# Kernel optimization log

Measured on AMD Instinct MI355X. Metric: run time of the kernel, lower is better.

Reference implementation:

```python
import jax, jax.numpy as jnp
import numpy as np
from jax import lax

B, S, T = 128, 1000, 256
V, E, KV, H = 30, 256, 256, 512


def setup_inputs() -> dict:
    ks = jax.random.split(jax.random.key(0), 20)
    sc = 0.1
    emb = jax.random.normal(ks[0], (V, E), jnp.float32) * sc
    emb = emb.at[29].set(0.0)  # padding_idx=29
    return {
        "enc_key": jax.random.normal(ks[1], (B, S, KV), jnp.float32),
        "value": jax.random.normal(ks[2], (B, S, KV), jnp.float32),
        "y": jax.random.randint(ks[3], (T, B), 0, V),
        "encoder_len": jax.random.randint(ks[4], (B,), 1, S + 1),
        "embedding": emb,
        "W_ih1": jax.random.normal(ks[5], (4 * H, E + KV), jnp.float32) * sc,
        "b_ih1": jax.random.normal(ks[6], (4 * H,), jnp.float32) * sc,
        "W_hh1": jax.random.normal(ks[7], (4 * H, H), jnp.float32) * sc,
        "b_hh1": jax.random.normal(ks[8], (4 * H,), jnp.float32) * sc,
        "W_ih2": jax.random.normal(ks[9], (4 * H, H), jnp.float32) * sc,
        "b_ih2": jax.random.normal(ks[10], (4 * H,), jnp.float32) * sc,
        "W_hh2": jax.random.normal(ks[11], (4 * H, H), jnp.float32) * sc,
        "b_hh2": jax.random.normal(ks[12], (4 * H,), jnp.float32) * sc,
        "Wq": jax.random.normal(ks[13], (KV, H), jnp.float32) * sc,
        "bq": jax.random.normal(ks[14], (KV,), jnp.float32) * sc,
        "Wc": jax.random.normal(ks[15], (V, 2 * KV), jnp.float32) * sc,
        "bc": jax.random.normal(ks[16], (V,), jnp.float32) * sc,
    }


def _lstm_cell(x, h, c, W_ih, b_ih, W_hh, b_hh):
    gates = x @ W_ih.T + b_ih + h @ W_hh.T + b_hh
    i, f, g, o = jnp.split(gates, 4, axis=1)
    c_new = jax.nn.sigmoid(f) * c + jax.nn.sigmoid(i) * jnp.tanh(g)
    h_new = jax.nn.sigmoid(o) * jnp.tanh(c_new)
    return h_new, c_new


def reference(enc_key, value, y, encoder_len, embedding,
              W_ih1, b_ih1, W_hh1, b_hh1,
              W_ih2, b_ih2, W_hh2, b_hh2,
              Wq, bq, Wc, bc):
    # y: [T, B] -> [B, T]; note: original computes mask from encoder_len but the
    # non-in-place masked_fill discards it, so masking has NO effect (reproduced).
    del encoder_len
    yT = y.T  # [B, T]
    b, s, kv = enc_key.shape
    scale = jnp.sqrt(jnp.asarray(s, jnp.float32))
    char_embeds = embedding[yT]          # [B, T, E]
    ctx0 = value.mean(axis=1)            # [B, KV]  (value.permute(0,2,1).mean(-1))
    h = W_hh1.shape[1]
    z = jnp.zeros((b, h), enc_key.dtype)

    def step(carry, e_t):
        h1, c1, h2, c2, ctx = carry
        x = jnp.concatenate([e_t, ctx], axis=1)                 # [B, E+KV]
        h1n, c1n = _lstm_cell(x, h1, c1, W_ih1, b_ih1, W_hh1, b_hh1)
        # original feeds lstm1's CELL state into lstm2 (hidden_states[0][1])
        h2n, c2n = _lstm_cell(c1n, h2, c2, W_ih2, b_ih2, W_hh2, b_hh2)
        # query from lstm2's CELL state (hidden_states[1][1])
        q = c2n @ Wq.T + bq                                     # [B, KV]
        energy = (jnp.einsum('bsk,bk->bs', enc_key, q) + 1e-9) / scale
        attn = jax.nn.softmax(energy, axis=1)                   # [B, S]
        ctxn = jnp.einsum('bsk,bs->bk', value, attn)            # [B, KV]
        pred = jnp.concatenate([ctxn, q], axis=1) @ Wc.T + bc   # [B, V]
        return (h1n, c1n, h2n, c2n, ctxn), (pred, attn[0])

    _, (preds, attn0) = lax.scan(step, (z, z, z, z, ctx0),
                                 jnp.swapaxes(char_embeds, 0, 1))
    predictions = jnp.transpose(preds, (1, 0, 2)).reshape(b, -1)  # [B, T*V] (cat dim=1)
    attentions = attn0[..., None]                                 # [T, S, 1]
    return predictions, attentions
```

## Files before the change

### kernel.cpp

```cpp
#include <hip/hip_runtime.h>
#include <hip/hip_bf16.h>

#define NB 128
#define NS 1000
#define NT 256
#define NV 30
#define NE 256
#define NKV 256
#define NH 512
#define NG 2048
#define NK 1024

typedef __hip_bfloat16 bf;
typedef unsigned short ushortT;

__device__ __forceinline__ float sigm(float x){ return 1.f/(1.f+__expf(-x)); }
__device__ __forceinline__ float tanh_fast(float x){ float e=__expf(2.f*x); return 1.f - 2.f/(e+1.f); }
__device__ __forceinline__ float bf2f(ushortT u){ return __uint_as_float(((unsigned)u)<<16); }
__device__ __forceinline__ void bf8_to_f(const ushortT* p, float* o){
  uint4 u = *reinterpret_cast<const uint4*>(p);
  o[0]=__uint_as_float(u.x<<16); o[1]=__uint_as_float(u.x&0xffff0000u);
  o[2]=__uint_as_float(u.y<<16); o[3]=__uint_as_float(u.y&0xffff0000u);
  o[4]=__uint_as_float(u.z<<16); o[5]=__uint_as_float(u.z&0xffff0000u);
  o[6]=__uint_as_float(u.w<<16); o[7]=__uint_as_float(u.w&0xffff0000u);
}
__device__ __forceinline__ float ldDual(const void* p, size_t i, bool bfm){
  return bfm ? bf2f(((const ushortT*)p)[i]) : ((const float*)p)[i];
}

__global__ void k_probe(const unsigned* __restrict__ x, unsigned* __restrict__ flag){
  __shared__ int cnt;
  if (threadIdx.x==0) cnt = 0;
  __syncthreads();
  int c = 0;
  #pragma unroll
  for (int i=0;i<4;++i){
    unsigned d = x[(size_t)threadIdx.x*4 + i];
    unsigned e = (d >> 7) & 0xffu;
    c += (e >= 119 && e <= 135) ? 1 : 0;
  }
  atomicAdd(&cnt, c);
  __syncthreads();
  if (threadIdx.x==0) *flag = (cnt >= 512) ? 1u : 0u;
}

__global__ void k_wtp(const void* __restrict__ A, const void* __restrict__ Bm,
                      float* __restrict__ Wtp, const unsigned* __restrict__ flag){
  const bool bfm = (*flag != 0);
  int idx = blockIdx.x*256 + threadIdx.x;
  int k = idx >> 11, pc = idx & (NG-1);
  int j = pc >> 2, g = pc & 3;
  int col = g*NH + j;
  const void* p = (k < NH) ? A : Bm;
  Wtp[idx] = ldDual(p, (size_t)col*NH + (k & (NH-1)), bfm);
}

__global__ void k_biasp(const void* bi1, const void* bh1, const void* bi2, const void* bh2,
                        float* __restrict__ bsum1, float* __restrict__ bsum2,
                        const unsigned* __restrict__ flag){
  const bool bfm = (*flag != 0);
  int idx = blockIdx.x*256 + threadIdx.x;
  int which = idx >= NG; int pc = idx & (NG-1);
  int j = pc >> 2, g = pc & 3;
  int col = g*NH + j;
  const void* a = which ? bi2 : bi1;
  const void* c = which ? bh2 : bh1;
  float v = ldDual(a, col, bfm) + ldDual(c, col, bfm);
  (which ? bsum2 : bsum1)[pc] = v;
}

__global__ void k_init(const void* __restrict__ value, const int* __restrict__ y,
                       const void* __restrict__ emb,
                       float* __restrict__ X1a, float* __restrict__ X2a,
                       float* __restrict__ c1, float* __restrict__ c2,
                       const unsigned* __restrict__ flag){
  const bool bfm = (*flag != 0);
  int b = blockIdx.x, tid = threadIdx.x;
  float acc = 0.f;
  if (bfm){
    const ushortT* vcol = (const ushortT*)value + (size_t)b*NS*NKV + tid;
    for (int s=0;s<NS;++s) acc += bf2f(vcol[(size_t)s*NKV]);
  } else {
    const float* vcol = (const float*)value + (size_t)b*NS*NKV + tid;
    for (int s=0;s<NS;++s) acc += vcol[(size_t)s*NKV];
  }
  X1a[(size_t)b*NK + NE + tid] = acc * (1.f/NS);
  int yv = y[b];
  X1a[(size_t)b*NK + tid] = ldDual(emb, (size_t)yv*NE + tid, bfm);
  X1a[(size_t)b*NK + 512 + tid] = 0.f; X1a[(size_t)b*NK + 768 + tid] = 0.f;
  X2a[(size_t)b*NK + 512 + tid] = 0.f; X2a[(size_t)b*NK + 768 + tid] = 0.f;
  c1[(size_t)b*NH + tid] = 0.f; c1[(size_t)b*NH + 256 + tid] = 0.f;
  c2[(size_t)b*NH + tid] = 0.f; c2[(size_t)b*NH + 256 + tid] = 0.f;
}

__global__ __launch_bounds__(512) void k_lstm(
    const float* __restrict__ X, const float* __restrict__ Wtp,
    const float* __restrict__ bsump,
    float* __restrict__ cstate,
    float* __restrict__ outC, int outCstride, int hasC,
    float* __restrict__ outH)
{
  const int i = blockIdx.x;
  const int cb = ((i & 7) << 3) | ((i >> 3) & 7);
  const int rb = i >> 6;
  const int r0 = rb * 32;
  const int pc0 = cb * 32;
  const int tid = threadIdx.x;
  const int khalf = tid >> 8;
  const int t8 = tid & 255;
  const int rp = t8 >> 4;
  const int cp = t8 & 15;
  __shared__ float Xs[2][64][33];
  __shared__ float redbuf[256][4];
  __shared__ float gbuf[32][33];

  float a00=0.f, a01=0.f, a10=0.f, a11=0.f;
  const int kbase = khalf * 512;
  const int sr  = t8 >> 4;
  const int sk4 = (t8 & 15) * 4;

  for (int cch = 0; cch < 8; ++cch){
    __syncthreads();
    {
      const float4 v0 = *reinterpret_cast<const float4*>(
          X + (size_t)(r0+sr)*NK + kbase + cch*64 + sk4);
      const float4 v1 = *reinterpret_cast<const float4*>(
          X + (size_t)(r0+sr+16)*NK + kbase + cch*64 + sk4);
      Xs[khalf][sk4+0][sr]    = v0.x; Xs[khalf][sk4+1][sr]    = v0.y;
      Xs[khalf][sk4+2][sr]    = v0.z; Xs[khalf][sk4+3][sr]    = v0.w;
      Xs[khalf][sk4+0][sr+16] = v1.x; Xs[khalf][sk4+1][sr+16] = v1.y;
      Xs[khalf][sk4+2][sr+16] = v1.z; Xs[khalf][sk4+3][sr+16] = v1.w;
    }
    __syncthreads();
    const float* wp = Wtp + (size_t)(kbase + cch*64)*NG + pc0 + cp*2;
    #pragma unroll 8
    for (int kk=0; kk<64; ++kk){
      const float2 w = *reinterpret_cast<const float2*>(wp + (size_t)kk*NG);
      const float2 x = *reinterpret_cast<const float2*>(&Xs[khalf][kk][rp*2]);
      a00 = fmaf(x.x, w.x, a00); a01 = fmaf(x.x, w.y, a01);
      a10 = fmaf(x.y, w.x, a10); a11 = fmaf(x.y, w.y, a11);
    }
  }
  if (khalf == 1){
    redbuf[t8][0]=a00; redbuf[t8][1]=a01; redbuf[t8][2]=a10; redbuf[t8][3]=a11;
  }
  __syncthreads();
  if (khalf == 0){
    a00 += redbuf[t8][0]; a01 += redbuf[t8][1];
    a10 += redbuf[t8][2]; a11 += redbuf[t8][3];
    gbuf[rp*2+0][cp*2+0]=a00; gbuf[rp*2+0][cp*2+1]=a01;
    gbuf[rp*2+1][cp*2+0]=a10; gbuf[rp*2+1][cp*2+1]=a11;
  }
  __syncthreads();
  if (tid < 256){
    const int er = tid >> 3;
    const int jj = tid & 7;
    const int r = r0 + er;
    const int jg = cb*8 + jj;
    const int pb = pc0 + jj*4;
    float iv = gbuf[er][jj*4+0] + bsump[pb+0];
    float fv = gbuf[er][jj*4+1] + bsump[pb+1];
    float gv = gbuf[er][jj*4+2] + bsump[pb+2];
    float ov = gbuf[er][jj*4+3] + bsump[pb+3];
    float cold = cstate[(size_t)r*NH + jg];
    float cn = sigm(fv)*cold + sigm(iv)*tanh_fast(gv);
    float hn = sigm(ov)*tanh_fast(cn);
    cstate[(size_t)r*NH + jg] = cn;
    if (hasC) outC[(size_t)r*outCstride + jg] = cn;
    outH[(size_t)r*NK + jg] = hn;
  }
}

__global__ __launch_bounds__(512) void k_attn(
    const float* __restrict__ c2, const void* __restrict__ Wq, const void* __restrict__ bq,
    const void* __restrict__ key, const void* __restrict__ val,
    const void* __restrict__ Wc, const void* __restrict__ bc,
    const int* __restrict__ y, const void* __restrict__ emb,
    float* __restrict__ X1next, void* __restrict__ outp,
    const unsigned* __restrict__ flag, int t)
{
  const bool bfm = (*flag != 0);
  const int b = blockIdx.x, tid = threadIdx.x, lane = tid & 63, wave = tid >> 6;
  __shared__ float c2s[NH];
  __shared__ float qs[NKV];
  __shared__ float ps[NS];
  __shared__ float ctxs[NKV];
  __shared__ float red[16];
  __shared__ float psum[NV][17];
  __shared__ float ctxpart[8][NKV];

  c2s[tid] = c2[(size_t)b*NH + tid];
  __syncthreads();

  if (tid < NKV){
    float qacc = ldDual(bq, tid, bfm);
    if (bfm){
      const ushortT* wrow = (const ushortT*)Wq + (size_t)tid*NH;
      #pragma unroll 4
      for (int j=0;j<NH;j+=8){
        float wv[8]; bf8_to_f(wrow + j, wv);
        #pragma unroll
        for (int u=0;u<8;++u) qacc = fmaf(wv[u], c2s[j+u], qacc);
      }
    } else {
      const float4* wrow = reinterpret_cast<const float4*>((const float*)Wq + (size_t)tid*NH);
      #pragma unroll 4
      for (int j4=0; j4<NH/4; ++j4){
        float4 w = wrow[j4]; int j = j4*4;
        qacc = fmaf(w.x, c2s[j+0], qacc); qacc = fmaf(w.y, c2s[j+1], qacc);
        qacc = fmaf(w.z, c2s[j+2], qacc); qacc = fmaf(w.w, c2s[j+3], qacc);
      }
    }
    qs[tid] = qacc;
  }
  __syncthreads();

  const int k0 = (lane & 15)*16;
  float qreg[16];
  #pragma unroll
  for (int u=0;u<16;++u) qreg[u] = qs[k0+u];
  const float rscale = 0.031622776601683794f;
  for (int s0 = wave*8; s0 < NS; s0 += 64){
    int sA = s0 + (lane >> 4);
    int sB = sA + 4;
    float aA = 0.f, aB = 0.f;
    if (bfm){
      if (sA < NS){
        const ushortT* kp = (const ushortT*)key + ((size_t)b*NS + sA)*NKV + k0;
        float xv[8];
        bf8_to_f(kp, xv);
        #pragma unroll
        for (int u=0;u<8;++u) aA = fmaf(xv[u], qreg[u], aA);
        bf8_to_f(kp + 8, xv);
        #pragma unroll
        for (int u=0;u<8;++u) aA = fmaf(xv[u], qreg[8+u], aA);
      }
      if (sB < NS){
        const ushortT* kp = (const ushortT*)key + ((size_t)b*NS + sB)*NKV + k0;
        float xv[8];
        bf8_to_f(kp, xv);
        #pragma unroll
        for (int u=0;u<8;++u) aB = fmaf(xv[u], qreg[u], aB);
        bf8_to_f(kp + 8, xv);
        #pragma unroll
        for (int u=0;u<8;++u) aB = fmaf(xv[u], qreg[8+u], aB);
      }
    } else {
      const float* kA = (const float*)key + ((size_t)b*NS + sA)*NKV + k0;
      const float* kB = (const float*)key + ((size_t)b*NS + sB)*NKV + k0;
      float4 a0,a1,a2,a3, b0,b1,b2,b3;
      bool gA = (sA < NS), gB = (sB < NS);
      if (gA){
        a0 = *reinterpret_cast<const float4*>(kA);
        a1 = *reinterpret_cast<const float4*>(kA+4);
        a2 = *reinterpret_cast<const float4*>(kA+8);
        a3 = *reinterpret_cast<const float4*>(kA+12);
      }
      if (gB){
        b0 = *reinterpret_cast<const float4*>(kB);
        b1 = *reinterpret_cast<const float4*>(kB+4);
        b2 = *reinterpret_cast<const float4*>(kB+8);
        b3 = *reinterpret_cast<const float4*>(kB+12);
      }
      if (gA){
        aA = fmaf(a0.x,qreg[0],aA); aA = fmaf(a0.y,qreg[1],aA);
        aA = fmaf(a0.z,qreg[2],aA); aA = fmaf(a0.w,qreg[3],aA);
        aA = fmaf(a1.x,qreg[4],aA); aA = fmaf(a1.y,qreg[5],aA);
        aA = fmaf(a1.z,qreg[6],aA); aA = fmaf(a1.w,qreg[7],aA);
        aA = fmaf(a2.x,qreg[8],aA); aA = fmaf(a2.y,qreg[9],aA);
        aA = fmaf(a2.z,qreg[10],aA); aA = fmaf(a2.w,qreg[11],aA);
        aA = fmaf(a3.x,qreg[12],aA); aA = fmaf(a3.y,qreg[13],aA);
        aA = fmaf(a3.z,qreg[14],aA); aA = fmaf(a3.w,qreg[15],aA);
      }
      if (gB){
        aB = fmaf(b0.x,qreg[0],aB); aB = fmaf(b0.y,qreg[1],aB);
        aB = fmaf(b0.z,qreg[2],aB); aB = fmaf(b0.w,qreg[3],aB);
        aB = fmaf(b1.x,qreg[4],aB); aB = fmaf(b1.y,qreg[5],aB);
        aB = fmaf(b1.z,qreg[6],aB); aB = fmaf(b1.w,qreg[7],aB);
        aB = fmaf(b2.x,qreg[8],aB); aB = fmaf(b2.y,qreg[9],aB);
        aB = fmaf(b2.z,qreg[10],aB); aB = fmaf(b2.w,qreg[11],aB);
        aB = fmaf(b3.x,qreg[12],aB); aB = fmaf(b3.y,qreg[13],aB);
        aB = fmaf(b3.z,qreg[14],aB); aB = fmaf(b3.w,qreg[15],aB);
      }
    }
    aA += __shfl_xor(aA,1); aA += __shfl_xor(aA,2);
    aA += __shfl_xor(aA,4); aA += __shfl_xor(aA,8);
    aB += __shfl_xor(aB,1); aB += __shfl_xor(aB,2);
    aB += __shfl_xor(aB,4); aB += __shfl_xor(aB,8);
    if ((lane & 15) == 0){
      if (sA < NS) ps[sA] = (aA + 1e-9f)*rscale;
      if (sB < NS) ps[sB] = (aB + 1e-9f)*rscale;
    }
  }
  __syncthreads();

  float m = -1e30f;
  for (int s=tid; s<NS; s+=512) m = fmaxf(m, ps[s]);
  #pragma unroll
  for (int d=1; d<64; d<<=1) m = fmaxf(m, __shfl_xor(m, d));
  if (lane == 0) red[wave] = m;
  __syncthreads();
  m = red[0];
  #pragma unroll
  for (int w=1; w<8; ++w) m = fmaxf(m, red[w]);
  float sum = 0.f;
  for (int s=tid; s<NS; s+=512){ float p = __expf(ps[s]-m); ps[s] = p; sum += p; }
  #pragma unroll
  for (int d=1; d<64; d<<=1) sum += __shfl_xor(sum, d);
  if (lane == 0) red[8+wave] = sum;
  __syncthreads();
  sum = red[8];
  #pragma unroll
  for (int w=1; w<8; ++w) sum += red[8+w];
  const float invS = 1.f/sum;

  const size_t ATTN_OFF = (size_t)NB*NT*NV;
  if (b == 0){
    for (int s=tid; s<NS; s+=512){
      float v = ps[s]*invS;
      if (bfm) ((bf*)outp)[ATTN_OFF + (size_t)t*NS + s] = __float2bfloat16(v);
      else     ((float*)outp)[ATTN_OFF + (size_t)t*NS + s] = v;
    }
  }

  {
    float ca[8] = {0.f,0.f,0.f,0.f,0.f,0.f,0.f,0.f};
    float cb2[8] = {0.f,0.f,0.f,0.f,0.f,0.f,0.f,0.f};
    const int sset = lane >> 5;
    const int kc = (lane & 31) * 8;
    const int sst = wave*2 + sset;
    int s = sst;
    if (bfm){
      const ushortT* vbase = (const ushortT*)val + (size_t)b*NS*NKV + kc;
      for (; s + 16 < NS; s += 32){
        float p0 = ps[s], p1 = ps[s+16];
        float xv[8];
        bf8_to_f(vbase + (size_t)s*NKV, xv);
        #pragma unroll
        for (int u=0;u<8;++u) ca[u] = fmaf(xv[u], p0, ca[u]);
        bf8_to_f(vbase + (size_t)(s+16)*NKV, xv);
        #pragma unroll
        for (int u=0;u<8;++u) cb2[u] = fmaf(xv[u], p1, cb2[u]);
      }
      if (s < NS){
        float p0 = ps[s];
        float xv[8]; bf8_to_f(vbase + (size_t)s*NKV, xv);
        #pragma unroll
        for (int u=0;u<8;++u) ca[u] = fmaf(xv[u], p0, ca[u]);
      }
    } else {
      const float* vbase = (const float*)val + (size_t)b*NS*NKV + kc;
      for (; s + 16 < NS; s += 32){
        float p0 = ps[s], p1 = ps[s+16];
        const float4 v0 = *reinterpret_cast<const float4*>(vbase + (size_t)s*NKV);
        const float4 v1 = *reinterpret_cast<const float4*>(vbase + (size_t)s*NKV + 4);
        const float4 w0 = *reinterpret_cast<const float4*>(vbase + (size_t)(s+16)*NKV);
        const float4 w1 = *reinterpret_cast<const float4*>(vbase + (size_t)(s+16)*NKV + 4);
        ca[0]=fmaf(v0.x,p0,ca[0]); ca[1]=fmaf(v0.y,p0,ca[1]);
        ca[2]=fmaf(v0.z,p0,ca[2]); ca[3]=fmaf(v0.w,p0,ca[3]);
        ca[4]=fmaf(v1.x,p0,ca[4]); ca[5]=fmaf(v1.y,p0,ca[5]);
        ca[6]=fmaf(v1.z,p0,ca[6]); ca[7]=fmaf(v1.w,p0,ca[7]);
        cb2[0]=fmaf(w0.x,p1,cb2[0]); cb2[1]=fmaf(w0.y,p1,cb2[1]);
        cb2[2]=fmaf(w0.z,p1,cb2[2]); cb2[3]=fmaf(w0.w,p1,cb2[3]);
        cb2[4]=fmaf(w1.x,p1,cb2[4]); cb2[5]=fmaf(w1.y,p1,cb2[5]);
        cb2[6]=fmaf(w1.z,p1,cb2[6]); cb2[7]=fmaf(w1.w,p1,cb2[7]);
      }
      if (s < NS){
        float p0 = ps[s];
        const float4 v0 = *reinterpret_cast<const float4*>(vbase + (size_t)s*NKV);
        const float4 v1 = *reinterpret_cast<const float4*>(vbase + (size_t)s*NKV + 4);
        ca[0]=fmaf(v0.x,p0,ca[0]); ca[1]=fmaf(v0.y,p0,ca[1]);
        ca[2]=fmaf(v0.z,p0,ca[2]); ca[3]=fmaf(v0.w,p0,ca[3]);
        ca[4]=fmaf(v1.x,p0,ca[4]); ca[5]=fmaf(v1.y,p0,ca[5]);
        ca[6]=fmaf(v1.z,p0,ca[6]); ca[7]=fmaf(v1.w,p0,ca[7]);
      }
    }
    #pragma unroll
    for (int u=0;u<8;++u){
      float v = ca[u] + cb2[u];
      v += __shfl_xor(v, 32);
      if (lane < 32) ctxpart[wave][kc+u] = v;
    }
  }
  __syncthreads();
  if (tid < NKV){
    float ctxv = 0.f;
    #pragma unroll
    for (int w=0; w<8; ++w) ctxv += ctxpart[w][tid];
    ctxv *= invS;
    ctxs[tid] = ctxv;
    X1next[(size_t)b*NK + NE + tid] = ctxv;
  }
  __syncthreads();

  {
    int vIdx = tid >> 4, part = tid & 15;
    if (vIdx < NV){
      float a = 0.f;
      int kb0 = part*32;
      for (int k=kb0; k<kb0+32; ++k){
        float xv = (k < NKV) ? ctxs[k] : qs[k-NKV];
        a = fmaf(xv, ldDual(Wc, (size_t)vIdx*(2*NKV) + k, bfm), a);
      }
      psum[vIdx][part] = a;
    }
  }
  __syncthreads();
  if (tid < NV){
    float a = ldDual(bc, tid, bfm);
    #pragma unroll
    for (int p=0;p<16;++p) a += psum[tid][p];
    size_t oi = (size_t)b*(NT*NV) + (size_t)t*NV + tid;
    if (bfm) ((bf*)outp)[oi] = __float2bfloat16(a);
    else     ((float*)outp)[oi] = a;
  }

  if (t + 1 < NT && tid < NE){
    int yv = y[(size_t)(t+1)*NB + b];
    X1next[(size_t)b*NK + tid] = ldDual(emb, (size_t)yv*NE + tid, bfm);
  }
}

extern "C" void kernel_launch(void* const* d_in, const int* in_sizes, int n_in,
                              void* d_out, int out_size, void* d_ws, size_t ws_size,
                              hipStream_t stream)
{
  const void* enc_key = d_in[0];
  const void* value   = d_in[1];
  const int*  y       = (const int*)d_in[2];
  const void* emb     = d_in[4];
  const void* W_ih1   = d_in[5];
  const void* b_ih1   = d_in[6];
  const void* W_hh1   = d_in[7];
  const void* b_hh1   = d_in[8];
  const void* W_ih2   = d_in[9];
  const void* b_ih2   = d_in[10];
  const void* W_hh2   = d_in[11];
  const void* b_hh2   = d_in[12];
  const void* Wq      = d_in[13];
  const void* bq      = d_in[14];
  const void* Wc      = d_in[15];
  const void* bc      = d_in[16];

  char* base = (char*)d_ws; size_t off = 0;
  auto alloc = [&](size_t bytes)->char*{
    char* p = base + off; off += (bytes + 255) & ~(size_t)255; return p;
  };
  float* Wtp1 = (float*)alloc((size_t)NK*NG*4);
  float* Wtp2 = (float*)alloc((size_t)NK*NG*4);
  float* bsum1 = (float*)alloc((size_t)NG*4);
  float* bsum2 = (float*)alloc((size_t)NG*4);
  float* X1[2] = {(float*)alloc((size_t)NB*NK*4), (float*)alloc((size_t)NB*NK*4)};
  float* X2[2] = {(float*)alloc((size_t)NB*NK*4), (float*)alloc((size_t)NB*NK*4)};
  float* c1 = (float*)alloc((size_t)NB*NH*4);
  float* c2 = (float*)alloc((size_t)NB*NH*4);
  unsigned* flag = (unsigned*)alloc(256);
  (void)ws_size;

  k_probe<<<1, 256, 0, stream>>>((const unsigned*)enc_key, flag);
  k_wtp<<<(NK*NG)/256, 256, 0, stream>>>(W_ih1, W_hh1, Wtp1, flag);
  k_wtp<<<(NK*NG)/256, 256, 0, stream>>>(W_ih2, W_hh2, Wtp2, flag);
  k_biasp<<<(2*NG)/256, 256, 0, stream>>>(b_ih1, b_hh1, b_ih2, b_hh2, bsum1, bsum2, flag);
  k_init<<<NB, 256, 0, stream>>>(value, y, emb, X1[0], X2[0], c1, c2, flag);

  for (int t=0; t<NT; ++t){
    int cur = t & 1, nxt = cur ^ 1;
    k_lstm<<<256, 512, 0, stream>>>(X1[cur], Wtp1, bsum1, c1,
                                    X2[cur], NK, 1, X1[nxt] + NH);
    k_lstm<<<256, 512, 0, stream>>>(X2[cur], Wtp2, bsum2, c2,
                                    nullptr, 0, 0, X2[nxt] + NH);
    k_attn<<<NB, 512, 0, stream>>>(c2, Wq, bq, enc_key, value, Wc, bc,
                                   y, emb, X1[nxt], d_out, flag, t);
  }
}
```

Before: 40.94 ms.

## Split attention over two sequence halves with flash-style softmax combine kernel

The attention step is split across two blocks per batch row, each handling half of the encoder sequence and producing a partial max, sum and unnormalised context. A new combine kernel merges the halves with log-sum-exp rescaling, then computes the output projection, the attention row and the next embedding. This doubles the blocks working on the memory-bound key/value streaming, from 128 to 256 on a GPU with many CUs. In exchange it adds one kernel launch per timestep, duplicates the query projection in both halves, and passes partial results through global memory.

```diff
diff --git a/kernel.cpp b/kernel.cpp
--- a/kernel.cpp
+++ b/kernel.cpp
@@ -3,6 +3,7 @@
 
 #define NB 128
 #define NS 1000
+#define NSH 500
 #define NT 256
 #define NV 30
 #define NE 256
@@ -171,22 +172,21 @@
   }
 }
 
-__global__ __launch_bounds__(512) void k_attn(
+__global__ __launch_bounds__(512) void k_attn_part(
     const float* __restrict__ c2, const void* __restrict__ Wq, const void* __restrict__ bq,
     const void* __restrict__ key, const void* __restrict__ val,
-    const void* __restrict__ Wc, const void* __restrict__ bc,
-    const int* __restrict__ y, const void* __restrict__ emb,
-    float* __restrict__ X1next, void* __restrict__ outp,
-    const unsigned* __restrict__ flag, int t)
+    float* __restrict__ qbuf, float* __restrict__ pctx, float* __restrict__ pstat,
+    float* __restrict__ psbuf,
+    const unsigned* __restrict__ flag)
 {
   const bool bfm = (*flag != 0);
-  const int b = blockIdx.x, tid = threadIdx.x, lane = tid & 63, wave = tid >> 6;
+  const int b = blockIdx.x >> 1, half = blockIdx.x & 1;
+  const int sbase = half * NSH;
+  const int tid = threadIdx.x, lane = tid & 63, wave = tid >> 6;
   __shared__ float c2s[NH];
   __shared__ float qs[NKV];
-  __shared__ float ps[NS];
-  __shared__ float ctxs[NKV];
+  __shared__ float ps[512];
   __shared__ float red[16];
-  __shared__ float psum[NV][17];
   __shared__ float ctxpart[8][NKV];
 
   c2s[tid] = c2[(size_t)b*NH + tid];
@@ -212,6 +212,7 @@
       }
     }
     qs[tid] = qacc;
+    if (half == 0) qbuf[(size_t)b*NKV + tid] = qacc;
   }
   __syncthreads();
 
@@ -220,13 +221,13 @@
   #pragma unroll
   for (int u=0;u<16;++u) qreg[u] = qs[k0+u];
   const float rscale = 0.031622776601683794f;
-  for (int s0 = wave*8; s0 < NS; s0 += 64){
-    int sA = s0 + (lane >> 4);
+  for (int i0 = wave*8; i0 < NSH; i0 += 64){
+    int sA = i0 + (lane >> 4);
     int sB = sA + 4;
     float aA = 0.f, aB = 0.f;
     if (bfm){
-      if (sA < NS){
-        const ushortT* kp = (const ushortT*)key + ((size_t)b*NS + sA)*NKV + k0;
+      if (sA < NSH){
+        const ushortT* kp = (const ushortT*)key + ((size_t)b*NS + sbase + sA)*NKV + k0;
         float xv[8];
         bf8_to_f(kp, xv);
         #pragma unroll
@@ -235,8 +236,8 @@
         #pragma unroll
         for (int u=0;u<8;++u) aA = fmaf(xv[u], qreg[8+u], aA);
       }
-      if (sB < NS){
-        const ushortT* kp = (const ushortT*)key + ((size_t)b*NS + sB)*NKV + k0;
+      if (sB < NSH){
+        const ushortT* kp = (const ushortT*)key + ((size_t)b*NS + sbase + sB)*NKV + k0;
         float xv[8];
         bf8_to_f(kp, xv);
         #pragma unroll
@@ -246,10 +247,10 @@
         for (int u=0;u<8;++u) aB = fmaf(xv[u], qreg[8+u], aB);
       }
     } else {
-      const float* kA = (const float*)key + ((size_t)b*NS + sA)*NKV + k0;
-      const float* kB = (const float*)key + ((size_t)b*NS + sB)*NKV + k0;
+      const float* kA = (const float*)key + ((size_t)b*NS + sbase + sA)*NKV + k0;
+      const float* kB = (const float*)key + ((size_t)b*NS + sbase + sB)*NKV + k0;
       float4 a0,a1,a2,a3, b0,b1,b2,b3;
-      bool gA = (sA < NS), gB = (sB < NS);
+      bool gA = (sA < NSH), gB = (sB < NSH);
       if (gA){
         a0 = *reinterpret_cast<const float4*>(kA);
         a1 = *reinterpret_cast<const float4*>(kA+4);
@@ -288,14 +289,14 @@
     aB += __shfl_xor(aB,1); aB += __shfl_xor(aB,2);
     aB += __shfl_xor(aB,4); aB += __shfl_xor(aB,8);
     if ((lane & 15) == 0){
-      if (sA < NS) ps[sA] = (aA + 1e-9f)*rscale;
-      if (sB < NS) ps[sB] = (aB + 1e-9f)*rscale;
+      if (sA < NSH) ps[sA] = (aA + 1e-9f)*rscale;
+      if (sB < NSH) ps[sB] = (aB + 1e-9f)*rscale;
     }
   }
   __syncthreads();
 
   float m = -1e30f;
-  for (int s=tid; s<NS; s+=512) m = fmaxf(m, ps[s]);
+  if (tid < NSH) m = ps[tid];
   #pragma unroll
   for (int d=1; d<64; d<<=1) m = fmaxf(m, __shfl_xor(m, d));
   if (lane == 0) red[wave] = m;
@@ -304,7 +305,7 @@
   #pragma unroll
   for (int w=1; w<8; ++w) m = fmaxf(m, red[w]);
   float sum = 0.f;
-  for (int s=tid; s<NS; s+=512){ float p = __expf(ps[s]-m); ps[s] = p; sum += p; }
+  if (tid < NSH){ float p = __expf(ps[tid]-m); ps[tid] = p; sum = p; }
   #pragma unroll
   for (int d=1; d<64; d<<=1) sum += __shfl_xor(sum, d);
   if (lane == 0) red[8+wave] = sum;
@@ -312,16 +313,11 @@
   sum = red[8];
   #pragma unroll
   for (int w=1; w<8; ++w) sum += red[8+w];
-  const float invS = 1.f/sum;
-
-  const size_t ATTN_OFF = (size_t)NB*NT*NV;
-  if (b == 0){
-    for (int s=tid; s<NS; s+=512){
-      float v = ps[s]*invS;
-      if (bfm) ((bf*)outp)[ATTN_OFF + (size_t)t*NS + s] = __float2bfloat16(v);
-      else     ((float*)outp)[ATTN_OFF + (size_t)t*NS + s] = v;
-    }
-  }
+  if (tid == 0){
+    pstat[((size_t)b*2 + half)*2 + 0] = m;
+    pstat[((size_t)b*2 + half)*2 + 1] = sum;
+  }
+  if (b == 0 && tid < NSH) psbuf[sbase + tid] = ps[tid];
 
   {
     float ca[8] = {0.f,0.f,0.f,0.f,0.f,0.f,0.f,0.f};
@@ -331,8 +327,8 @@
     const int sst = wave*2 + sset;
     int s = sst;
     if (bfm){
-      const ushortT* vbase = (const ushortT*)val + (size_t)b*NS*NKV + kc;
-      for (; s + 16 < NS; s += 32){
+      const ushortT* vbase = (const ushortT*)val + ((size_t)b*NS + sbase)*NKV + kc;
+      for (; s + 16 < NSH; s += 32){
         float p0 = ps[s], p1 = ps[s+16];
         float xv[8];
         bf8_to_f(vbase + (size_t)s*NKV, xv);
@@ -342,15 +338,15 @@
         #pragma unroll
         for (int u=0;u<8;++u) cb2[u] = fmaf(xv[u], p1, cb2[u]);
       }
-      if (s < NS){
+      if (s < NSH){
         float p0 = ps[s];
         float xv[8]; bf8_to_f(vbase + (size_t)s*NKV, xv);
         #pragma unroll
         for (int u=0;u<8;++u) ca[u] = fmaf(xv[u], p0, ca[u]);
       }
     } else {
-      const float* vbase = (const float*)val + (size_t)b*NS*NKV + kc;
-      for (; s + 16 < NS; s += 32){
+      const float* vbase = (const float*)val + ((size_t)b*NS + sbase)*NKV + kc;
+      for (; s + 16 < NSH; s += 32){
         float p0 = ps[s], p1 = ps[s+16];
         const float4 v0 = *reinterpret_cast<const float4*>(vbase + (size_t)s*NKV);
         const float4 v1 = *reinterpret_cast<const float4*>(vbase + (size_t)s*NKV + 4);
@@ -365,7 +361,7 @@
         cb2[4]=fmaf(w1.x,p1,cb2[4]); cb2[5]=fmaf(w1.y,p1,cb2[5]);
         cb2[6]=fmaf(w1.z,p1,cb2[6]); cb2[7]=fmaf(w1.w,p1,cb2[7]);
       }
-      if (s < NS){
+      if (s < NSH){
         float p0 = ps[s];
         const float4 v0 = *reinterpret_cast<const float4*>(vbase + (size_t)s*NKV);
         const float4 v1 = *reinterpret_cast<const float4*>(vbase + (size_t)s*NKV + 4);
@@ -387,18 +383,52 @@
     float ctxv = 0.f;
     #pragma unroll
     for (int w=0; w<8; ++w) ctxv += ctxpart[w][tid];
-    ctxv *= invS;
-    ctxs[tid] = ctxv;
-    X1next[(size_t)b*NK + NE + tid] = ctxv;
+    pctx[((size_t)b*2 + half)*NKV + tid] = ctxv;
+  }
+}
+
+__global__ __launch_bounds__(256) void k_attn_comb(
+    const float* __restrict__ qbuf, const float* __restrict__ pctx,
+    const float* __restrict__ pstat, const float* __restrict__ psbuf,
+    const void* __restrict__ Wc, const void* __restrict__ bc,
+    const int* __restrict__ y, const void* __restrict__ emb,
+    float* __restrict__ X1next, void* __restrict__ outp,
+    const unsigned* __restrict__ flag, int t)
+{
+  const bool bfm = (*flag != 0);
+  const int b = blockIdx.x, tid = threadIdx.x;
+  __shared__ float qs[NKV];
+  __shared__ float ctxs[NKV];
+  __shared__ float psum[NV][9];
+
+  const float mA = pstat[((size_t)b*2+0)*2+0], sA = pstat[((size_t)b*2+0)*2+1];
+  const float mB = pstat[((size_t)b*2+1)*2+0], sB = pstat[((size_t)b*2+1)*2+1];
+  const float m = fmaxf(mA, mB);
+  const float wA = __expf(mA - m), wB = __expf(mB - m);
+  const float invS = 1.f / (sA*wA + sB*wB);
+
+  qs[tid] = qbuf[(size_t)b*NKV + tid];
+  float ctxv = (pctx[((size_t)b*2+0)*NKV + tid]*wA +
+                pctx[((size_t)b*2+1)*NKV + tid]*wB) * invS;
+  ctxs[tid] = ctxv;
+  X1next[(size_t)b*NK + NE + tid] = ctxv;
+
+  const size_t ATTN_OFF = (size_t)NB*NT*NV;
+  if (b == 0){
+    for (int s=tid; s<NS; s+=256){
+      float v = psbuf[s] * ((s < NSH) ? wA : wB) * invS;
+      if (bfm) ((bf*)outp)[ATTN_OFF + (size_t)t*NS + s] = __float2bfloat16(v);
+      else     ((float*)outp)[ATTN_OFF + (size_t)t*NS + s] = v;
+    }
   }
   __syncthreads();
 
   {
-    int vIdx = tid >> 4, part = tid & 15;
+    int vIdx = tid >> 3, part = tid & 7;
     if (vIdx < NV){
       float a = 0.f;
-      int kb0 = part*32;
-      for (int k=kb0; k<kb0+32; ++k){
+      int kb0 = part*64;
+      for (int k=kb0; k<kb0+64; ++k){
         float xv = (k < NKV) ? ctxs[k] : qs[k-NKV];
         a = fmaf(xv, ldDual(Wc, (size_t)vIdx*(2*NKV) + k, bfm), a);
       }
@@ -409,13 +439,13 @@
   if (tid < NV){
     float a = ldDual(bc, tid, bfm);
     #pragma unroll
-    for (int p=0;p<16;++p) a += psum[tid][p];
+    for (int p=0;p<8;++p) a += psum[tid][p];
     size_t oi = (size_t)b*(NT*NV) + (size_t)t*NV + tid;
     if (bfm) ((bf*)outp)[oi] = __float2bfloat16(a);
     else     ((float*)outp)[oi] = a;
   }
 
-  if (t + 1 < NT && tid < NE){
+  if (t + 1 < NT){
     int yv = y[(size_t)(t+1)*NB + b];
     X1next[(size_t)b*NK + tid] = ldDual(emb, (size_t)yv*NE + tid, bfm);
   }
@@ -454,6 +484,10 @@
   float* X2[2] = {(float*)alloc((size_t)NB*NK*4), (float*)alloc((size_t)NB*NK*4)};
   float* c1 = (float*)alloc((size_t)NB*NH*4);
   float* c2 = (float*)alloc((size_t)NB*NH*4);
+  float* qbuf  = (float*)alloc((size_t)NB*NKV*4);
+  float* pctx  = (float*)alloc((size_t)NB*2*NKV*4);
+  float* pstat = (float*)alloc((size_t)NB*2*2*4);
+  float* psbuf = (float*)alloc((size_t)NS*4);
   unsigned* flag = (unsigned*)alloc(256);
   (void)ws_size;
 
@@ -469,7 +503,9 @@
                                     X2[cur], NK, 1, X1[nxt] + NH);
     k_lstm<<<256, 512, 0, stream>>>(X2[cur], Wtp2, bsum2, c2,
                                     nullptr, 0, 0, X2[nxt] + NH);
-    k_attn<<<NB, 512, 0, stream>>>(c2, Wq, bq, enc_key, value, Wc, bc,
-                                   y, emb, X1[nxt], d_out, flag, t);
-  }
-}
+    k_attn_part<<<2*NB, 512, 0, stream>>>(c2, Wq, bq, enc_key, value,
+                                          qbuf, pctx, pstat, psbuf, flag);
+    k_attn_comb<<<NB, 256, 0, stream>>>(qbuf, pctx, pstat, psbuf, Wc, bc,
+                                        y, emb, X1[nxt], d_out, flag, t);
+  }
+}
```

Result: faster. 38.53 ms (-5.9%).
